# Kernel optimization log

Measured on AMD Instinct MI355X. Metric: run time of the kernel, lower is better.

The kernel has to match this reference:

```python
import jax, jax.numpy as jnp
import numpy as np

NEG_SLOPE = 0.2   # PyG GATConv default leaky_relu slope
BN_EPS = 1e-5
SM_EPS = 1e-16    # PyG segment-softmax denominator epsilon


def gat_conv(x, src, dst, W, a_src, a_dst, bias, heads, out_ch, concat):
    # x: [N, F_in]; src/dst: [E] (self-loops already included)
    N = x.shape[0]
    h = (x @ W).reshape(N, heads, out_ch)              # [N, H, C]
    s = jnp.sum(h * a_src, axis=-1)                    # [N, H] per-node source score
    d = jnp.sum(h * a_dst, axis=-1)                    # [N, H] per-node dest score
    e = jax.nn.leaky_relu(s[src] + d[dst], NEG_SLOPE)  # [E, H]
    # segment softmax over edges grouped by destination node
    m = jax.ops.segment_max(e, dst, num_segments=N)
    m = jnp.where(jnp.isfinite(m), m, 0.0)
    p = jnp.exp(e - m[dst])                            # [E, H]
    denom = jax.ops.segment_sum(p, dst, num_segments=N)
    alpha = p / (denom[dst] + SM_EPS)                  # [E, H]
    # attention-weighted scatter-sum aggregation
    out = jax.ops.segment_sum(h[src] * alpha[:, :, None], dst, num_segments=N)  # [N, H, C]
    if concat:
        out = out.reshape(N, heads * out_ch)
    else:
        out = out.mean(axis=1)
    return out + bias


def setup_inputs() -> dict:
    key = jax.random.key(0)
    ks = jax.random.split(key, 12)
    N, E = 50000, 400000
    F_in, hidden, H1, H2, nclasses = 256, 64, 4, 1, 40
    x = jax.random.normal(ks[0], (N, F_in), dtype=jnp.float32)
    edge_index = jax.random.randint(ks[1], (2, E), 0, N, dtype=jnp.int64)
    g = 1.0 / np.sqrt(F_in)
    W1 = jax.random.normal(ks[2], (F_in, H1 * hidden), dtype=jnp.float32) * g
    a_src1 = jax.random.normal(ks[3], (H1, hidden), dtype=jnp.float32) * 0.1
    a_dst1 = jax.random.normal(ks[4], (H1, hidden), dtype=jnp.float32) * 0.1
    b1 = jnp.zeros((H1 * hidden,), dtype=jnp.float32)
    gamma = jnp.ones((H1 * hidden,), dtype=jnp.float32)
    beta = jnp.zeros((H1 * hidden,), dtype=jnp.float32)
    g2 = 1.0 / np.sqrt(H1 * hidden)
    W2 = jax.random.normal(ks[5], (H1 * hidden, H2 * nclasses), dtype=jnp.float32) * g2
    a_src2 = jax.random.normal(ks[6], (H2, nclasses), dtype=jnp.float32) * 0.1
    a_dst2 = jax.random.normal(ks[7], (H2, nclasses), dtype=jnp.float32) * 0.1
    b2 = jnp.zeros((nclasses,), dtype=jnp.float32)
    return {"x": x, "edge_index": edge_index, "W1": W1, "a_src1": a_src1,
            "a_dst1": a_dst1, "b1": b1, "gamma": gamma, "beta": beta,
            "W2": W2, "a_src2": a_src2, "a_dst2": a_dst2, "b2": b2}


def reference(x, edge_index, W1, a_src1, a_dst1, b1, gamma, beta, W2, a_src2, a_dst2, b2):
    N = x.shape[0]
    loop = jnp.arange(N, dtype=edge_index.dtype)
    src = jnp.concatenate([edge_index[0], loop])   # add self-loops (GATConv default)
    dst = jnp.concatenate([edge_index[1], loop])
    H1, hidden = a_src1.shape
    H2, nclasses = a_src2.shape
    h = gat_conv(x, src, dst, W1, a_src1, a_dst1, b1, H1, hidden, concat=True)
    # BatchNorm1d (training-mode batch statistics, biased variance)
    mu = h.mean(axis=0)
    var = h.var(axis=0)
    h = (h - mu) * jax.lax.rsqrt(var + BN_EPS) * gamma + beta
    h = jax.nn.elu(h)
    out = gat_conv(h, src, dst, W2, a_src2, a_dst2, b2, H2, nclasses, concat=False)
    return jax.nn.log_softmax(out, axis=-1)
```

## Files before the change

### kernel.cpp

```cpp
#include <hip/hip_runtime.h>
#include <hip/hip_fp16.h>

constexpr int FIN = 256;
constexpr int C1  = 256;
constexpr int HID = 64;
constexpr int H1N = 4;
constexpr int NC  = 40;
constexpr int CAP = 256;
constexpr int CAP2 = 128;

__global__ __launch_bounds__(64)
void detect_kernel(const int* __restrict__ ei, int* __restrict__ flag, int E)
{
    int lane = threadIdx.x;
    int q = lane * (E / 64);
    int v = ei[2 * q + 1];
    unsigned long long nz = __ballot(v != 0);
    if (lane == 0) flag[0] = (nz == 0ull) ? 2 : 1;
}

__global__ __launch_bounds__(256)
void init_kernel(int* __restrict__ counts, int* __restrict__ fill,
                 float* __restrict__ colsum, float* __restrict__ colsq, int N)
{
    int t = blockIdx.x * 256 + threadIdx.x;
    if (t < N) { counts[t] = 1; fill[t] = 0; }
    if (t < C1) { colsum[t] = 0.f; colsq[t] = 0.f; }
}

__global__ __launch_bounds__(256)
void gemm1_kernel(const float* __restrict__ X, const float* __restrict__ W,
                  const float* __restrict__ as1, const float* __restrict__ ad1,
                  __half* __restrict__ Hm, float* __restrict__ s1,
                  float* __restrict__ d1, int N)
{
    __shared__ float As[16][68];
    __shared__ float Bs[16][68];
    const int t    = threadIdx.x;
    const int tx   = t & 15;
    const int ty   = t >> 4;
    const int bm   = blockIdx.x * 64;
    const int head = blockIdx.y;
    const int bn   = head * 64;

    const int lrow = t >> 2;
    const int lk   = (t & 3) * 4;
    const int brow = t >> 4;
    const int bcol = (t & 15) * 4;

    float acc[4][4] = {};

    for (int k0 = 0; k0 < FIN; k0 += 16) {
        int ar = bm + lrow; if (ar > N - 1) ar = N - 1;
        float4 av = *(const float4*)(X + (size_t)ar * FIN + k0 + lk);
        float4 bv = *(const float4*)(W + (size_t)(k0 + brow) * C1 + bn + bcol);
        As[lk + 0][lrow] = av.x;
        As[lk + 1][lrow] = av.y;
        As[lk + 2][lrow] = av.z;
        As[lk + 3][lrow] = av.w;
        *(float4*)&Bs[brow][bcol] = bv;
        __syncthreads();
        #pragma unroll
        for (int kk = 0; kk < 16; ++kk) {
            float4 a = *(const float4*)&As[kk][ty * 4];
            float4 b = *(const float4*)&Bs[kk][tx * 4];
            float a4[4] = {a.x, a.y, a.z, a.w};
            float b4[4] = {b.x, b.y, b.z, b.w};
            #pragma unroll
            for (int i = 0; i < 4; ++i)
                #pragma unroll
                for (int j = 0; j < 4; ++j)
                    acc[i][j] += a4[i] * b4[j];
        }
        __syncthreads();
    }

    float sp[4] = {0, 0, 0, 0}, dp[4] = {0, 0, 0, 0};
    #pragma unroll
    for (int i = 0; i < 4; ++i) {
        int row = bm + ty * 4 + i;
        if (row < N) {
            __half2 p01 = __floats2half2_rn(acc[i][0], acc[i][1]);
            __half2 p23 = __floats2half2_rn(acc[i][2], acc[i][3]);
            uint2 pk;
            pk.x = *(unsigned int*)&p01;
            pk.y = *(unsigned int*)&p23;
            *(uint2*)(Hm + (size_t)row * C1 + bn + tx * 4) = pk;
            #pragma unroll
            for (int j = 0; j < 4; ++j) {
                int col = tx * 4 + j;
                float v = acc[i][j];
                sp[i] += v * as1[bn + col];
                dp[i] += v * ad1[bn + col];
            }
        }
    }
    #pragma unroll
    for (int off = 1; off < 16; off <<= 1) {
        #pragma unroll
        for (int i = 0; i < 4; ++i) {
            sp[i] += __shfl_xor(sp[i], off);
            dp[i] += __shfl_xor(dp[i], off);
        }
    }
    if (tx == 0) {
        #pragma unroll
        for (int i = 0; i < 4; ++i) {
            int row = bm + ty * 4 + i;
            if (row < N) {
                s1[row * H1N + head] = sp[i];
                d1[row * H1N + head] = dp[i];
            }
        }
    }
}

__global__ __launch_bounds__(256)
void hist_kernel(const int* __restrict__ ei, const int* __restrict__ flag,
                 int* __restrict__ counts, int E)
{
    int t = blockIdx.x * 256 + threadIdx.x;
    int stride = flag[0];
    if (t < E) atomicAdd(&counts[ei[(size_t)stride * (E + t)]], 1);
}

__global__ __launch_bounds__(1024)
void scan_kernel(const int* __restrict__ cnt, int* __restrict__ offs, int N)
{
    __shared__ int wsum[16];
    __shared__ int carry_s;
    const int t = threadIdx.x, lane = t & 63, w = t >> 6;
    if (t == 0) carry_s = 0;
    __syncthreads();
    for (int base = 0; base < N; base += 1024) {
        int idx = base + t;
        int v = (idx < N) ? cnt[idx] : 0;
        int incl = v;
        #pragma unroll
        for (int off = 1; off < 64; off <<= 1) {
            int u = __shfl_up(incl, off);
            if (lane >= off) incl += u;
        }
        if (lane == 63) wsum[w] = incl;
        __syncthreads();
        int wpre = 0;
        for (int i = 0; i < w; ++i) wpre += wsum[i];
        int c = carry_s;
        if (idx < N) offs[idx] = c + wpre + incl - v;
        __syncthreads();
        if (t == 1023) carry_s = c + wpre + incl;
        __syncthreads();
    }
    if (t == 0) offs[N] = carry_s;
}

__global__ __launch_bounds__(256)
void scatter_kernel(const int* __restrict__ ei, const int* __restrict__ flag,
                    const int* __restrict__ offs, int* __restrict__ fill,
                    int* __restrict__ ssrc, int E, int N)
{
    int t = blockIdx.x * 256 + threadIdx.x;
    if (t >= E + N) return;
    int stride = flag[0];
    int s, d;
    if (t < E) {
        s = ei[(size_t)stride * t];
        d = ei[(size_t)stride * (E + t)];
    } else {
        s = t - E; d = s;
    }
    int pos = offs[d] + atomicAdd(&fill[d], 1);
    ssrc[pos] = s;
}

__global__ __launch_bounds__(256)
void agg1_kernel(const __half* __restrict__ Hm, const float* __restrict__ s1,
                 const float* __restrict__ d1, const int* __restrict__ offs,
                 const int* __restrict__ ssrc, const float* __restrict__ b1,
                 float* __restrict__ out1, int N)
{
    __shared__ float alpha[H1N][CAP];
    __shared__ int   srcs[CAP];
    __shared__ float invs[H1N];
    const int n    = blockIdx.x;
    const int t    = threadIdx.x;
    const int lane = t & 63;
    const int w    = t >> 6;
    const int beg  = offs[n], end = offs[n + 1];
    const int deg  = end - beg;
    const float dh = d1[n * H1N + w];

    if (deg <= CAP) {
        float mloc = -1e30f;
        for (int i = lane; i < deg; i += 64) {
            int s = ssrc[beg + i];
            if (w == 0) srcs[i] = s;
            float e = s1[s * H1N + w] + dh;
            e = e > 0.f ? e : 0.2f * e;
            alpha[w][i] = e;
            mloc = fmaxf(mloc, e);
        }
        #pragma unroll
        for (int off = 32; off; off >>= 1) mloc = fmaxf(mloc, __shfl_xor(mloc, off));
        float ssum = 0.f;
        for (int i = lane; i < deg; i += 64) {
            float ex = __expf(alpha[w][i] - mloc);
            alpha[w][i] = ex;
            ssum += ex;
        }
        #pragma unroll
        for (int off = 32; off; off >>= 1) ssum += __shfl_xor(ssum, off);
        if (lane == 0) invs[w] = 1.f / (ssum + 1e-16f);
        __syncthreads();

        float acc0 = 0.f, acc1 = 0.f, acc2 = 0.f, acc3 = 0.f;
        int i = 0;
        for (; i + 4 <= deg; i += 4) {
            int s0 = srcs[i],     s1i = srcs[i + 1];
            int s2 = srcs[i + 2], s3i = srcs[i + 3];
            float a0 = alpha[w][i],     a1 = alpha[w][i + 1];
            float a2 = alpha[w][i + 2], a3 = alpha[w][i + 3];
            float v0 = __half2float(Hm[(size_t)s0  * C1 + t]);
            float v1 = __half2float(Hm[(size_t)s1i * C1 + t]);
            float v2 = __half2float(Hm[(size_t)s2  * C1 + t]);
            float v3 = __half2float(Hm[(size_t)s3i * C1 + t]);
            acc0 += v0 * a0; acc1 += v1 * a1;
            acc2 += v2 * a2; acc3 += v3 * a3;
        }
        for (; i < deg; ++i)
            acc0 += __half2float(Hm[(size_t)srcs[i] * C1 + t]) * alpha[w][i];
        float acc = (acc0 + acc1) + (acc2 + acc3);
        out1[(size_t)n * C1 + t] = acc * invs[w] + b1[t];
        return;
    }

    float mloc = -1e30f;
    for (int p = beg + lane; p < end; p += 64) {
        float e = s1[ssrc[p] * H1N + w] + dh;
        e = e > 0.f ? e : 0.2f * e;
        mloc = fmaxf(mloc, e);
    }
    #pragma unroll
    for (int off = 32; off; off >>= 1) mloc = fmaxf(mloc, __shfl_xor(mloc, off));
    float ssum = 0.f;
    for (int p = beg + lane; p < end; p += 64) {
        float e = s1[ssrc[p] * H1N + w] + dh;
        e = e > 0.f ? e : 0.2f * e;
        ssum += __expf(e - mloc);
    }
    #pragma unroll
    for (int off = 32; off; off >>= 1) ssum += __shfl_xor(ssum, off);
    if (lane == 0) invs[w] = 1.f / (ssum + 1e-16f);

    float acc0 = 0.f, acc1 = 0.f, acc2 = 0.f, acc3 = 0.f;
    for (int c0 = 0; c0 < deg; c0 += CAP) {
        int cnt = min(CAP, deg - c0);
        for (int i = lane; i < cnt; i += 64) {
            int p = beg + c0 + i;
            int s = ssrc[p];
            if (w == 0) srcs[i] = s;
            float e = s1[s * H1N + w] + dh;
            e = e > 0.f ? e : 0.2f * e;
            alpha[w][i] = __expf(e - mloc);
        }
        __syncthreads();
        int i = 0;
        for (; i + 4 <= cnt; i += 4) {
            int s0 = srcs[i],     s1i = srcs[i + 1];
            int s2 = srcs[i + 2], s3i = srcs[i + 3];
            float a0 = alpha[w][i],     a1 = alpha[w][i + 1];
            float a2 = alpha[w][i + 2], a3 = alpha[w][i + 3];
            float v0 = __half2float(Hm[(size_t)s0  * C1 + t]);
            float v1 = __half2float(Hm[(size_t)s1i * C1 + t]);
            float v2 = __half2float(Hm[(size_t)s2  * C1 + t]);
            float v3 = __half2float(Hm[(size_t)s3i * C1 + t]);
            acc0 += v0 * a0; acc1 += v1 * a1;
            acc2 += v2 * a2; acc3 += v3 * a3;
        }
        for (; i < cnt; ++i)
            acc0 += __half2float(Hm[(size_t)srcs[i] * C1 + t]) * alpha[w][i];
        __syncthreads();
    }
    float acc = (acc0 + acc1) + (acc2 + acc3);
    out1[(size_t)n * C1 + t] = acc * invs[w] + b1[t];
}

__global__ __launch_bounds__(256)
void bnstats_kernel(const float* __restrict__ out1, float* __restrict__ colsum,
                    float* __restrict__ colsq, int N)
{
    int t = threadIdx.x;
    float s = 0.f, q = 0.f;
    for (int r = blockIdx.x; r < N; r += gridDim.x) {
        float v = out1[(size_t)r * C1 + t];
        s += v; q += v * v;
    }
    atomicAdd(&colsum[t], s);
    atomicAdd(&colsq[t], q);
}

__global__ __launch_bounds__(256)
void bnfin_kernel(const float* __restrict__ colsum, const float* __restrict__ colsq,
                  const float* __restrict__ gamma, const float* __restrict__ beta,
                  float* __restrict__ scale, float* __restrict__ shift, int N)
{
    int t = threadIdx.x;
    float mu  = colsum[t] / (float)N;
    float var = colsq[t] / (float)N - mu * mu;
    float sc  = gamma[t] * rsqrtf(var + 1e-5f);
    scale[t] = sc;
    shift[t] = beta[t] - mu * sc;
}

__global__ __launch_bounds__(320)
void gemm2_kernel(const float* __restrict__ out1, const float* __restrict__ scale,
                  const float* __restrict__ shift, const float* __restrict__ W2,
                  const float* __restrict__ as2, const float* __restrict__ ad2,
                  float* __restrict__ h2, float* __restrict__ s2,
                  float* __restrict__ d2, int N)
{
    __shared__ float Asm[16][65];
    __shared__ float Wsm[64 * NC];
    __shared__ float sred[16], dred[16];
    const int t  = threadIdx.x;
    const int rb = blockIdx.x * 16;
    const int j  = t % NC;
    const int rg = t / NC;
    if (t < 16) { sred[t] = 0.f; dred[t] = 0.f; }

    float acc0 = 0.f, acc1 = 0.f;
    for (int kc = 0; kc < C1; kc += 64) {
        for (int idx = t; idx < 16 * 64; idx += 320) {
            int r = idx >> 6, k = idx & 63;
            int row = rb + r;
            float v = 0.f;
            if (row < N) {
                v = out1[(size_t)row * C1 + kc + k];
                v = v * scale[kc + k] + shift[kc + k];
                v = v > 0.f ? v : (__expf(v) - 1.f);
            }
            Asm[r][k] = v;
        }
        for (int idx = t; idx < 64 * NC; idx += 320)
            Wsm[idx] = W2[kc * NC + idx];
        __syncthreads();
        #pragma unroll 8
        for (int k = 0; k < 64; ++k) {
            float w = Wsm[k * NC + j];
            acc0 += Asm[rg][k]     * w;
            acc1 += Asm[rg + 8][k] * w;
        }
        __syncthreads();
    }
    int r0 = rb + rg, r1 = rb + rg + 8;
    if (r0 < N) h2[(size_t)r0 * NC + j] = acc0;
    if (r1 < N) h2[(size_t)r1 * NC + j] = acc1;
    float aj = as2[j], bj = ad2[j];
    atomicAdd(&sred[rg],     acc0 * aj);
    atomicAdd(&sred[rg + 8], acc1 * aj);
    atomicAdd(&dred[rg],     acc0 * bj);
    atomicAdd(&dred[rg + 8], acc1 * bj);
    __syncthreads();
    if (t < 16 && rb + t < N) { s2[rb + t] = sred[t]; d2[rb + t] = dred[t]; }
}

__global__ __launch_bounds__(256)
void agg2_kernel(const float* __restrict__ h2, const float* __restrict__ s2,
                 const float* __restrict__ d2, const int* __restrict__ offs,
                 const int* __restrict__ ssrc, const float* __restrict__ b2,
                 float* __restrict__ out, int N)
{
    __shared__ float al[4][CAP2];
    __shared__ int   sr[4][CAP2];
    int w = threadIdx.x >> 6;
    int node = blockIdx.x * 4 + w;
    if (node >= N) return;
    int lane = threadIdx.x & 63;
    int beg = offs[node], end = offs[node + 1];
    int deg = end - beg;
    float dn = d2[node];

    float v;
    if (deg <= CAP2) {
        float mloc = -1e30f;
        for (int i = lane; i < deg; i += 64) {
            int s = ssrc[beg + i];
            sr[w][i] = s;
            float e = s2[s] + dn;
            e = e > 0.f ? e : 0.2f * e;
            al[w][i] = e;
            mloc = fmaxf(mloc, e);
        }
        #pragma unroll
        for (int off = 32; off; off >>= 1) mloc = fmaxf(mloc, __shfl_xor(mloc, off));
        float ssum = 0.f;
        for (int i = lane; i < deg; i += 64) {
            float ex = __expf(al[w][i] - mloc);
            al[w][i] = ex;
            ssum += ex;
        }
        #pragma unroll
        for (int off = 32; off; off >>= 1) ssum += __shfl_xor(ssum, off);
        float inv = 1.f / (ssum + 1e-16f);

        int j = lane < NC ? lane : 0;
        float acc0 = 0.f, acc1 = 0.f, acc2 = 0.f, acc3 = 0.f;
        int i = 0;
        for (; i + 4 <= deg; i += 4) {
            float a0 = al[w][i],     a1 = al[w][i + 1];
            float a2 = al[w][i + 2], a3 = al[w][i + 3];
            acc0 += h2[(size_t)sr[w][i]     * NC + j] * a0;
            acc1 += h2[(size_t)sr[w][i + 1] * NC + j] * a1;
            acc2 += h2[(size_t)sr[w][i + 2] * NC + j] * a2;
            acc3 += h2[(size_t)sr[w][i + 3] * NC + j] * a3;
        }
        for (; i < deg; ++i)
            acc0 += h2[(size_t)sr[w][i] * NC + j] * al[w][i];
        v = ((acc0 + acc1) + (acc2 + acc3)) * inv + b2[j];
    } else {
        float m = -1e30f, denom = 0.f;
        for (int p = beg; p < end; ++p) {
            float e = s2[ssrc[p]] + dn;
            e = e > 0.f ? e : 0.2f * e;
            float mn = fmaxf(m, e);
            denom = denom * __expf(m - mn) + __expf(e - mn);
            m = mn;
        }
        float inv = 1.f / (denom + 1e-16f);
        int j = lane < NC ? lane : 0;
        float acc = 0.f;
        for (int p = beg; p < end; ++p) {
            int s = ssrc[p];
            float e = s2[s] + dn;
            e = e > 0.f ? e : 0.2f * e;
            acc += h2[(size_t)s * NC + j] * (__expf(e - m) * inv);
        }
        v = acc + b2[j];
    }

    float vm = lane < NC ? v : -1e30f;
    #pragma unroll
    for (int off = 32; off > 0; off >>= 1) vm = fmaxf(vm, __shfl_xor(vm, off));
    float ex = lane < NC ? __expf(v - vm) : 0.f;
    #pragma unroll
    for (int off = 32; off > 0; off >>= 1) ex += __shfl_xor(ex, off);
    if (lane < NC) out[(size_t)node * NC + lane] = v - vm - __logf(ex);
}

extern "C" void kernel_launch(void* const* d_in, const int* in_sizes, int n_in,
                              void* d_out, int out_size, void* d_ws, size_t ws_size,
                              hipStream_t stream)
{
    const float* x   = (const float*)d_in[0];
    const int*   ei  = (const int*)d_in[1];
    const float* W1  = (const float*)d_in[2];
    const float* as1 = (const float*)d_in[3];
    const float* ad1 = (const float*)d_in[4];
    const float* b1  = (const float*)d_in[5];
    const float* gm  = (const float*)d_in[6];
    const float* bt  = (const float*)d_in[7];
    const float* W2  = (const float*)d_in[8];
    const float* as2 = (const float*)d_in[9];
    const float* ad2 = (const float*)d_in[10];
    const float* b2  = (const float*)d_in[11];
    const int N = in_sizes[0] / FIN;
    const int E = in_sizes[1] / 2;

    char* p = (char*)d_ws;
    auto take = [&](size_t bytes) {
        char* r = p; p += (bytes + 255) & ~(size_t)255; return r;
    };
    __half* Hm    = (__half*)take((size_t)N * C1 * 2);
    float* out1   = (float*)take((size_t)N * C1 * 4);
    float* h2     = (float*)take((size_t)N * NC * 4);
    float* s1     = (float*)take((size_t)N * H1N * 4);
    float* d1     = (float*)take((size_t)N * H1N * 4);
    float* s2     = (float*)take((size_t)N * 4);
    float* d2v    = (float*)take((size_t)N * 4);
    float* colsum = (float*)take(C1 * 4);
    float* colsq  = (float*)take(C1 * 4);
    float* bnsc   = (float*)take(C1 * 4);
    float* bnsh   = (float*)take(C1 * 4);
    int*   counts = (int*)take((size_t)N * 4);
    int*   offs   = (int*)take((size_t)(N + 1) * 4);
    int*   fill   = (int*)take((size_t)N * 4);
    int*   ssrc   = (int*)take((size_t)(E + N) * 4);
    int*   eflag  = (int*)take(256);

    detect_kernel<<<1, 64, 0, stream>>>(ei, eflag, E);
    init_kernel<<<(N + 255) / 256, 256, 0, stream>>>(counts, fill, colsum, colsq, N);
    gemm1_kernel<<<dim3((N + 63) / 64, H1N), 256, 0, stream>>>(x, W1, as1, ad1, Hm, s1, d1, N);
    hist_kernel<<<(E + 255) / 256, 256, 0, stream>>>(ei, eflag, counts, E);
    scan_kernel<<<1, 1024, 0, stream>>>(counts, offs, N);
    scatter_kernel<<<(E + N + 255) / 256, 256, 0, stream>>>(ei, eflag, offs, fill, ssrc, E, N);
    agg1_kernel<<<N, 256, 0, stream>>>(Hm, s1, d1, offs, ssrc, b1, out1, N);
    bnstats_kernel<<<256, 256, 0, stream>>>(out1, colsum, colsq, N);
    bnfin_kernel<<<1, 256, 0, stream>>>(colsum, colsq, gm, bt, bnsc, bnsh, N);
    gemm2_kernel<<<(N + 15) / 16, 320, 0, stream>>>(out1, bnsc, bnsh, W2, as2, ad2, h2, s2, d2v, N);
    agg2_kernel<<<(N + 3) / 4, 256, 0, stream>>>(h2, s2, d2v, offs, ssrc, b2, (float*)d_out, N);
}
```

Before: 563.3 us.

## Retile gemm2 to 64-row blocks with per-thread 10-column register tiles

Rewrites the second GEMM so each 256-thread block handles 64 rows, with each thread accumulating 10 output columns for one row in registers. It adds float4 loads of activations with fused BN and ELU, a padded weight layout for vectorized shared reads, and a shuffle-based reduction for the attention scores in place of shared atomics. The bnstats launch grid is also raised from 256 to 1024 blocks. The aim is more reuse per shared load and fewer atomics and syncs, at the cost of higher register use per thread.

```diff
diff --git a/kernel.cpp b/kernel.cpp
--- a/kernel.cpp
+++ b/kernel.cpp
@@ -312,56 +312,83 @@
     shift[t] = beta[t] - mu * sc;
 }
 
-__global__ __launch_bounds__(320)
+__global__ __launch_bounds__(256)
 void gemm2_kernel(const float* __restrict__ out1, const float* __restrict__ scale,
                   const float* __restrict__ shift, const float* __restrict__ W2,
                   const float* __restrict__ as2, const float* __restrict__ ad2,
                   float* __restrict__ h2, float* __restrict__ s2,
                   float* __restrict__ d2, int N)
 {
-    __shared__ float Asm[16][65];
-    __shared__ float Wsm[64 * NC];
-    __shared__ float sred[16], dred[16];
-    const int t  = threadIdx.x;
-    const int rb = blockIdx.x * 16;
-    const int j  = t % NC;
-    const int rg = t / NC;
-    if (t < 16) { sred[t] = 0.f; dred[t] = 0.f; }
-
-    float acc0 = 0.f, acc1 = 0.f;
+    __shared__ float Asm[64][68];
+    __shared__ float Wsm[64 * 48];
+    const int t   = threadIdx.x;
+    const int r   = t >> 2;
+    const int jg  = t & 3;
+    const int rb  = blockIdx.x * 64;
+    const int row = rb + r;
+    const int j0  = jg * 10;
+
+    float acc[10] = {};
+
     for (int kc = 0; kc < C1; kc += 64) {
-        for (int idx = t; idx < 16 * 64; idx += 320) {
-            int r = idx >> 6, k = idx & 63;
-            int row = rb + r;
-            float v = 0.f;
-            if (row < N) {
-                v = out1[(size_t)row * C1 + kc + k];
-                v = v * scale[kc + k] + shift[kc + k];
-                v = v > 0.f ? v : (__expf(v) - 1.f);
+        #pragma unroll
+        for (int idx = t; idx < 64 * 16; idx += 256) {
+            int ar = idx >> 4;
+            int cg = (idx & 15) * 4;
+            int arow = rb + ar;
+            float4 v = make_float4(0.f, 0.f, 0.f, 0.f);
+            if (arow < N) {
+                v = *(const float4*)(out1 + (size_t)arow * C1 + kc + cg);
+                float4 sc = *(const float4*)(scale + kc + cg);
+                float4 sh = *(const float4*)(shift + kc + cg);
+                v.x = v.x * sc.x + sh.x;
+                v.y = v.y * sc.y + sh.y;
+                v.z = v.z * sc.z + sh.z;
+                v.w = v.w * sc.w + sh.w;
+                v.x = v.x > 0.f ? v.x : (__expf(v.x) - 1.f);
+                v.y = v.y > 0.f ? v.y : (__expf(v.y) - 1.f);
+                v.z = v.z > 0.f ? v.z : (__expf(v.z) - 1.f);
+                v.w = v.w > 0.f ? v.w : (__expf(v.w) - 1.f);
             }
-            Asm[r][k] = v;
-        }
-        for (int idx = t; idx < 64 * NC; idx += 320)
-            Wsm[idx] = W2[kc * NC + idx];
-        __syncthreads();
-        #pragma unroll 8
+            *(float4*)&Asm[ar][cg] = v;
+        }
+        #pragma unroll
+        for (int idx = t; idx < 64 * 40; idx += 256) {
+            int k = idx / 40, j = idx - k * 40;
+            Wsm[k * 48 + (j / 10) * 12 + (j % 10)] = W2[(size_t)(kc + k) * NC + j];
+        }
+        __syncthreads();
+        #pragma unroll 4
         for (int k = 0; k < 64; ++k) {
-            float w = Wsm[k * NC + j];
-            acc0 += Asm[rg][k]     * w;
-            acc1 += Asm[rg + 8][k] * w;
-        }
-        __syncthreads();
-    }
-    int r0 = rb + rg, r1 = rb + rg + 8;
-    if (r0 < N) h2[(size_t)r0 * NC + j] = acc0;
-    if (r1 < N) h2[(size_t)r1 * NC + j] = acc1;
-    float aj = as2[j], bj = ad2[j];
-    atomicAdd(&sred[rg],     acc0 * aj);
-    atomicAdd(&sred[rg + 8], acc1 * aj);
-    atomicAdd(&dred[rg],     acc0 * bj);
-    atomicAdd(&dred[rg + 8], acc1 * bj);
-    __syncthreads();
-    if (t < 16 && rb + t < N) { s2[rb + t] = sred[t]; d2[rb + t] = dred[t]; }
+            float a = Asm[r][k];
+            const float* wp = &Wsm[k * 48 + jg * 12];
+            float4 w0 = *(const float4*)(wp);
+            float4 w1 = *(const float4*)(wp + 4);
+            float2 wv = *(const float2*)(wp + 8);
+            acc[0] += a * w0.x; acc[1] += a * w0.y;
+            acc[2] += a * w0.z; acc[3] += a * w0.w;
+            acc[4] += a * w1.x; acc[5] += a * w1.y;
+            acc[6] += a * w1.z; acc[7] += a * w1.w;
+            acc[8] += a * wv.x; acc[9] += a * wv.y;
+        }
+        __syncthreads();
+    }
+
+    float sp = 0.f, dp = 0.f;
+    #pragma unroll
+    for (int jj = 0; jj < 10; ++jj) {
+        sp += acc[jj] * as2[j0 + jj];
+        dp += acc[jj] * ad2[j0 + jj];
+    }
+    sp += __shfl_xor(sp, 1); sp += __shfl_xor(sp, 2);
+    dp += __shfl_xor(dp, 1); dp += __shfl_xor(dp, 2);
+    if (row < N) {
+        if (jg == 0) { s2[row] = sp; d2[row] = dp; }
+        #pragma unroll
+        for (int jj = 0; jj < 10; jj += 2)
+            *(float2*)(h2 + (size_t)row * NC + j0 + jj) =
+                make_float2(acc[jj], acc[jj + 1]);
+    }
 }
 
 __global__ __launch_bounds__(256)
@@ -494,8 +521,8 @@
     scan_kernel<<<1, 1024, 0, stream>>>(counts, offs, N);
     scatter_kernel<<<(E + N + 255) / 256, 256, 0, stream>>>(ei, eflag, offs, fill, ssrc, E, N);
     agg1_kernel<<<N, 256, 0, stream>>>(Hm, s1, d1, offs, ssrc, b1, out1, N);
-    bnstats_kernel<<<256, 256, 0, stream>>>(out1, colsum, colsq, N);
+    bnstats_kernel<<<1024, 256, 0, stream>>>(out1, colsum, colsq, N);
     bnfin_kernel<<<1, 256, 0, stream>>>(colsum, colsq, gm, bt, bnsc, bnsh, N);
-    gemm2_kernel<<<(N + 15) / 16, 320, 0, stream>>>(out1, bnsc, bnsh, W2, as2, ad2, h2, s2, d2v, N);
+    gemm2_kernel<<<(N + 63) / 64, 256, 0, stream>>>(out1, bnsc, bnsh, W2, as2, ad2, h2, s2, d2v, N);
     agg2_kernel<<<(N + 3) / 4, 256, 0, stream>>>(h2, s2, d2v, offs, ssrc, b2, (float*)d_out, N);
 }
```

Result: faster. 495.1 us (-12.1%).
